# Kernel optimization log

Measured on AMD Instinct MI355X. Metric: run time of the kernel, lower is better.

The kernel has to match this reference:

```python
import jax, jax.numpy as jnp
import numpy as np

B, N, T, C, H, E = 4, 256, 36, 64, 4, 4096
D = C // H          # per-head dim
CH = 2 * C          # GAT hidden channels (embed_size * 2)


def _ln(x, g, b):
    mu = x.mean(-1, keepdims=True)
    v = ((x - mu) ** 2).mean(-1, keepdims=True)
    return (x - mu) / jnp.sqrt(v + 1e-5) * g + b


def _gat_conv(x, src, dst, W, a_s, a_d, b):
    # GATConv, heads=1, add_self_loops=False, negative_slope=0.2
    h = x @ W                                        # [N, F]
    e = jax.nn.leaky_relu((h * a_s).sum(-1)[src] + (h * a_d).sum(-1)[dst], 0.2)  # [E]
    m = jax.ops.segment_max(e, dst, num_segments=N)  # per-dst softmax (stable)
    w = jnp.exp(e - m[dst])
    s = jax.ops.segment_sum(w, dst, num_segments=N)
    alpha = w / (s[dst] + 1e-16)
    return jax.ops.segment_sum(h[src] * alpha[:, None], dst, num_segments=N) + b


def _forward(query, key, value, edge_attr, D_S, W_emb, b_emb, Wq, Wk, Wv, W_fc, b_fc,
             ln1_g, ln1_b, ln2_g, ln2_b, W_ff1, b_ff1, W_ff2, b_ff2,
             gat1_W, gat1_as, gat1_ad, gat1_b, gat2_W, gat2_as, gat2_ad, gat2_b,
             jk_W, jk_b, W_fs, b_fs, W_fg, b_fg, edge_index):
    src, dst = edge_index[0], edge_index[1]

    def gat(x):  # [N, C] -> [N, C]; 2-layer GAT with jk='max'
        h1 = jax.nn.relu(_gat_conv(x, src, dst, gat1_W, gat1_as, gat1_ad, gat1_b))
        h2 = jax.nn.relu(_gat_conv(h1, src, dst, gat2_W, gat2_as, gat2_ad, gat2_b))
        return jnp.maximum(h1, h2) @ jk_W + jk_b

    # GAT is applied to the ORIGINAL query (before D_S is added), once per timestep.
    xg = jax.vmap(jax.vmap(gat))(query.transpose(0, 2, 1, 3))  # [B, T, N, C]
    # source loop PREPENDS each timestep's output -> time axis is reversed
    X_G = xg[:, ::-1].transpose(0, 2, 1, 3)                    # [B, N, T, C]

    ds = (D_S @ W_emb + b_emb)[None, :, None, :]               # [1, N, 1, C]
    q = query + ds
    k = key + ds
    v = value + ds

    qh = q.reshape(B, N, T, H, D) @ Wq                         # per-head shared linear
    kh = k.reshape(B, N, T, H, D) @ Wk
    vh = v.reshape(B, N, T, H, D) @ Wv
    attn = jnp.einsum('bqthd,bkthd->bqkth', qh, kh)            # [B, N, N, T, H]
    # NOTE: source softmaxes over dim=1 (the QUERY axis), scaled by sqrt(embed_size)
    a = jax.nn.softmax(attn / jnp.sqrt(jnp.float32(C)), axis=1)
    o = jnp.einsum('bqkth,bkthd->bqthd', a, vh).reshape(B, N, T, C)
    o = o @ W_fc + b_fc

    M_s = _ln(o + q, ln1_g, ln1_b)                             # dropout p=0 (identity)
    ff = jax.nn.relu(M_s @ W_ff1 + b_ff1) @ W_ff2 + b_ff2
    U_s = _ln(ff + M_s, ln2_g, ln2_b)

    g = jax.nn.sigmoid(U_s @ W_fs + b_fs + X_G @ W_fg + b_fg)
    return g * U_s + (1.0 - g) * X_G


def setup_inputs():
    key = jax.random.key(0)
    ki = iter(jax.random.split(key, 64))

    def p(shape):
        fan = shape[0]
        return jax.random.normal(next(ki), shape, dtype=jnp.float32) / jnp.float32(float(np.sqrt(fan)))

    inp = {}
    inp['query'] = jax.random.normal(next(ki), (B, N, T, C), dtype=jnp.float32)
    inp['key'] = jax.random.normal(next(ki), (B, N, T, C), dtype=jnp.float32)
    inp['value'] = jax.random.normal(next(ki), (B, N, T, C), dtype=jnp.float32)
    inp['edge_attr'] = jax.random.normal(next(ki), (E,), dtype=jnp.float32)
    inp['D_S'] = jax.random.normal(next(ki), (N, N), dtype=jnp.float32)  # adj, learned param
    inp['W_emb'] = p((N, C)); inp['b_emb'] = jnp.zeros((C,), jnp.float32)
    inp['Wq'] = p((D, D)); inp['Wk'] = p((D, D)); inp['Wv'] = p((D, D))
    inp['W_fc'] = p((C, C)); inp['b_fc'] = jnp.zeros((C,), jnp.float32)
    inp['ln1_g'] = jnp.ones((C,), jnp.float32); inp['ln1_b'] = jnp.zeros((C,), jnp.float32)
    inp['ln2_g'] = jnp.ones((C,), jnp.float32); inp['ln2_b'] = jnp.zeros((C,), jnp.float32)
    inp['W_ff1'] = p((C, 4 * C)); inp['b_ff1'] = jnp.zeros((4 * C,), jnp.float32)
    inp['W_ff2'] = p((4 * C, C)); inp['b_ff2'] = jnp.zeros((C,), jnp.float32)
    inp['gat1_W'] = p((C, CH)); inp['gat1_as'] = p((CH,)); inp['gat1_ad'] = p((CH,)); inp['gat1_b'] = jnp.zeros((CH,), jnp.float32)
    inp['gat2_W'] = p((CH, CH)); inp['gat2_as'] = p((CH,)); inp['gat2_ad'] = p((CH,)); inp['gat2_b'] = jnp.zeros((CH,), jnp.float32)
    inp['jk_W'] = p((CH, C)); inp['jk_b'] = jnp.zeros((C,), jnp.float32)
    inp['W_fs'] = p((C, C)); inp['b_fs'] = jnp.zeros((C,), jnp.float32)
    inp['W_fg'] = p((C, C)); inp['b_fg'] = jnp.zeros((C,), jnp.float32)
    inp['edge_index'] = jax.random.randint(next(ki), (2, E), 0, N, dtype=jnp.int32)
    return inp


def reference(query, key, value, edge_attr, D_S, W_emb, b_emb, Wq, Wk, Wv, W_fc, b_fc,
              ln1_g, ln1_b, ln2_g, ln2_b, W_ff1, b_ff1, W_ff2, b_ff2,
              gat1_W, gat1_as, gat1_ad, gat1_b, gat2_W, gat2_as, gat2_ad, gat2_b,
              jk_W, jk_b, W_fs, b_fs, W_fg, b_fg, edge_index):
    return _forward(query, key, value, edge_attr, D_S, W_emb, b_emb, Wq, Wk, Wv, W_fc, b_fc,
                    ln1_g, ln1_b, ln2_g, ln2_b, W_ff1, b_ff1, W_ff2, b_ff2,
                    gat1_W, gat1_as, gat1_ad, gat1_b, gat2_W, gat2_as, gat2_ad, gat2_b,
                    jk_W, jk_b, W_fs, b_fs, W_fg, b_fg, edge_index)
```

## Files before the change

### kernel.cpp

```cpp
#include <hip/hip_runtime.h>

typedef unsigned short u16;
typedef unsigned int u32;

#define B_ 4
#define N_ 256
#define T_ 36
#define C_ 64
#define H_ 4
#define D_ 16
#define CH_ 128
#define E_ 4096
#define EQ_ 1408
#define G_ (B_*T_)
#define TOK_ (B_*N_*T_)

#define DS_OFF  0
#define XG_OFF  (DS_OFF + N_*C_)
#define HA_OFF  (XG_OFF + TOK_*C_)
#define HB_OFF  (HA_OFF + G_*N_*CH_/2)
#define HS_OFF  (HB_OFF + G_*N_*CH_/2)
#define HD_OFF  (HS_OFF + G_*N_)
#define INT_OFF (HD_OFF + G_*N_)
#define MS_OFF  (INT_OFF + 4608)
#define O_SEP_OFF (MS_OFF + 576*512)

__device__ __forceinline__ float bf2f(u16 u){
  u32 x = ((u32)u) << 16;
  return __builtin_bit_cast(float, x);
}
__device__ __forceinline__ u16 f2bf(float f){
  u32 x = __builtin_bit_cast(u32, f);
  x += 0x7fffu + ((x >> 16) & 1u);
  return (u16)(x >> 16);
}
__device__ __forceinline__ void unpack8(uint4 u, float* f){
  f[0]=bf2f((u16)(u.x & 0xffffu)); f[1]=bf2f((u16)(u.x >> 16));
  f[2]=bf2f((u16)(u.y & 0xffffu)); f[3]=bf2f((u16)(u.y >> 16));
  f[4]=bf2f((u16)(u.z & 0xffffu)); f[5]=bf2f((u16)(u.z >> 16));
  f[6]=bf2f((u16)(u.w & 0xffffu)); f[7]=bf2f((u16)(u.w >> 16));
}
__device__ __forceinline__ uint4 pack8f(const float* f){
  uint4 u;
  u.x = (u32)f2bf(f[0]) | ((u32)f2bf(f[1]) << 16);
  u.y = (u32)f2bf(f[2]) | ((u32)f2bf(f[3]) << 16);
  u.z = (u32)f2bf(f[4]) | ((u32)f2bf(f[5]) << 16);
  u.w = (u32)f2bf(f[6]) | ((u32)f2bf(f[7]) << 16);
  return u;
}
__device__ __forceinline__ int rfl(int v){ return __builtin_amdgcn_readfirstlane(v); }

__device__ __forceinline__ void gq_from_bid(int bid, int& g, int& q){
  int xc = bid & 7, slot = bid >> 3;
  q = slot & 3;
  g = xc + ((slot >> 2) << 3);
}

#define SP_ 20

__device__ __forceinline__ void edge_softmax_par(int tid, int n0,
    const int* __restrict__ indptr, int p00,
    const int* srcs_l, const float* hs_l, const float* __restrict__ hd_ws,
    int g, float* alpha_l)
{
  const int ld = tid >> 2;
  const int sl = tid & 3;
  const int dst = n0 + ld;
  const int p0 = indptr[dst] - p00, p1 = indptr[dst+1] - p00;
  const float hdn = hd_ws[g*N_ + dst];
  float m = -1e30f;
  for (int j = p0 + sl; j < p1; j += 4){
    float e = hs_l[srcs_l[j]] + hdn;
    e = e > 0.f ? e : 0.2f * e;
    alpha_l[j] = e;
    m = fmaxf(m, e);
  }
  m = fmaxf(m, __shfl_xor(m, 1, 64));
  m = fmaxf(m, __shfl_xor(m, 2, 64));
  float s = 0.f;
  for (int j = p0 + sl; j < p1; j += 4){
    float w = __expf(alpha_l[j] - m);
    alpha_l[j] = w; s += w;
  }
  s += __shfl_xor(s, 1, 64);
  s += __shfl_xor(s, 2, 64);
  float inv = 1.f / (s + 1e-16f);
  for (int j = p0 + sl; j < p1; j += 4) alpha_l[j] *= inv;
}

__global__ __launch_bounds__(256)
void k_pre(const float* __restrict__ query, const float* __restrict__ W1,
           const float* __restrict__ as1, const float* __restrict__ ad1,
           u16* __restrict__ h, float* __restrict__ hs_ws, float* __restrict__ hd_ws,
           const float* __restrict__ DSm, const float* __restrict__ Wemb,
           const float* __restrict__ bemb, float* __restrict__ dsb,
           const int* __restrict__ ei, int* __restrict__ indptr, int* __restrict__ srcs)
{
  __shared__ union UP {
    struct { float xs[64][65]; float red[2][4][64]; } lin;
    struct { int srcL[E_]; int dstL[E_]; int tmp[E_]; int cnt[N_]; int base[N_+1]; } c;
  } S;
  const int bid = blockIdx.x;
  const int tid = threadIdx.x;

  if (bid < 576){
    int g, q; gq_from_bid(bid, g, q);
    const int n0 = q * 64;
    const int b = g / T_, t = g % T_;
    {
      const size_t gb = (((size_t)b*N_ + n0)*T_ + t)*C_;
      #pragma unroll
      for (int it = 0; it < 4; it++){
        int idx = tid + 256*it;
        int row = idx >> 4, c4 = (idx & 15) * 4;
        float4 v = *(const float4*)(query + gb + (size_t)row*(T_*C_) + c4);
        S.lin.xs[row][c4+0] = v.x; S.lin.xs[row][c4+1] = v.y;
        S.lin.xs[row][c4+2] = v.z; S.lin.xs[row][c4+3] = v.w;
      }
    }
    __syncthreads();

    const int r = tid & 63;
    const int cb = rfl(tid >> 6);
    const int ch0 = cb * 32;

    float acc[32];
    #pragma unroll
    for (int j = 0; j < 32; j++) acc[j] = 0.f;
    for (int k = 0; k < 64; k++){
      float xv = S.lin.xs[r][k];
      const float* wrow = W1 + k*CH_ + ch0;
      #pragma unroll
      for (int j = 0; j < 32; j++) acc[j] += xv * wrow[j];
    }
    float hs = 0.f, hd = 0.f;
    #pragma unroll
    for (int j = 0; j < 32; j++){ hs += acc[j]*as1[ch0+j]; hd += acc[j]*ad1[ch0+j]; }
    S.lin.red[0][cb][r] = hs; S.lin.red[1][cb][r] = hd;

    u16* hp = h + ((size_t)(g*N_ + n0 + r))*CH_ + ch0;
    #pragma unroll
    for (int j8 = 0; j8 < 32; j8 += 8)
      *(uint4*)(hp + j8) = pack8f(&acc[j8]);

    __syncthreads();
    if (tid < 64){
      float a = S.lin.red[0][0][tid]+S.lin.red[0][1][tid]+S.lin.red[0][2][tid]+S.lin.red[0][3][tid];
      float d = S.lin.red[1][0][tid]+S.lin.red[1][1][tid]+S.lin.red[1][2][tid]+S.lin.red[1][3][tid];
      hs_ws[g*N_ + n0 + tid] = a;
      hd_ws[g*N_ + n0 + tid] = d;
    }
  } else if (bid < 640){
    const int n = (bid - 576) * 4 + (tid >> 6);
    const int c = tid & 63;
    float acc = bemb[c];
    for (int m = 0; m < N_; m++) acc += DSm[n*N_ + m] * Wemb[m*C_ + c];
    dsb[n*C_ + c] = acc;
  } else {
    for (int e = tid; e < E_; e += 256){ S.c.srcL[e] = ei[e]; S.c.dstL[e] = ei[E_ + e]; }
    S.c.cnt[tid] = 0;
    __syncthreads();
    for (int e = tid; e < E_; e += 256) atomicAdd(&S.c.cnt[S.c.dstL[e]], 1);
    __syncthreads();
    if (tid == 0){
      int run = 0;
      for (int i = 0; i < N_; i++){ S.c.base[i] = run; run += S.c.cnt[i]; }
      S.c.base[N_] = run;
    }
    __syncthreads();
    S.c.cnt[tid] = 0;
    __syncthreads();
    for (int e = tid; e < E_; e += 256){
      int d = S.c.dstL[e];
      int p = atomicAdd(&S.c.cnt[d], 1);
      S.c.tmp[S.c.base[d] + p] = e;
    }
    __syncthreads();
    {
      const int p0 = S.c.base[tid], p1 = S.c.base[tid] + S.c.cnt[tid];
      for (int i = p0 + 1; i < p1; i++){
        int v = S.c.tmp[i]; int j = i - 1;
        while (j >= p0 && S.c.tmp[j] > v){ S.c.tmp[j+1] = S.c.tmp[j]; j--; }
        S.c.tmp[j+1] = v;
      }
      for (int j = p0; j < p1; j++) srcs[j] = S.c.srcL[S.c.tmp[j]];
    }
    indptr[tid] = S.c.base[tid];
    if (tid == 0) indptr[N_] = S.c.base[N_];
  }
}

__global__ __launch_bounds__(256)
void k_agg1stat(const u16* __restrict__ hin, const float* __restrict__ hs_ws, const float* __restrict__ hd_ws,
                const int* __restrict__ indptr, const int* __restrict__ srcs,
                const float* __restrict__ bias, u16* __restrict__ hout,
                const float* __restrict__ query, const float* __restrict__ key,
                const float* __restrict__ Wq, const float* __restrict__ Wk,
                const float* __restrict__ dsb, float* __restrict__ mS)
{
  __shared__ union UA {
    struct { int srcs_l[EQ_]; float alpha_l[EQ_]; float hs_l[N_]; } a;
    struct { float qs[N_][SP_]; float wq[16][16]; float wk[16][16]; } s;
  } U;
  const int bid = blockIdx.x;
  const int tid = threadIdx.x;

  if (bid < 576){
    int g, q; gq_from_bid(bid, g, q);
    const int n0 = q * 64;

    const int p00 = indptr[n0];
    const int pend = indptr[n0 + 64];
    const int cntE = pend - p00;
    for (int i = tid; i < cntE; i += 256) U.a.srcs_l[i] = srcs[p00 + i];
    U.a.hs_l[tid] = hs_ws[g*N_ + tid];
    __syncthreads();

    edge_softmax_par(tid, n0, indptr, p00, U.a.srcs_l, U.a.hs_l, hd_ws, g, U.a.alpha_l);
    __syncthreads();

    const int r = tid & 63;
    const int cb = rfl(tid >> 6);
    const int ch0 = cb * 32;
    const int dst = n0 + r;
    const int p0 = indptr[dst] - p00, p1 = indptr[dst+1] - p00;

    float acc[32];
    #pragma unroll
    for (int j = 0; j < 32; j++) acc[j] = 0.f;
    for (int j = p0; j < p1; j++){
      float a = U.a.alpha_l[j];
      int s = U.a.srcs_l[j];
      const uint4* hp = (const uint4*)(hin + ((size_t)(g*N_ + s))*CH_ + ch0);
      #pragma unroll
      for (int qq = 0; qq < 4; qq++){
        float hv[8]; unpack8(hp[qq], hv);
        #pragma unroll
        for (int i = 0; i < 8; i++) acc[qq*8+i] += a * hv[i];
      }
    }
    float o[32];
    #pragma unroll
    for (int j = 0; j < 32; j++){
      float v = acc[j] + bias[ch0+j];
      o[j] = v > 0.f ? v : 0.f;
    }
    u16* op = hout + ((size_t)(g*N_ + dst))*CH_ + ch0;
    #pragma unroll
    for (int j8 = 0; j8 < 32; j8 += 8)
      *(uint4*)(op + j8) = pack8f(&o[j8]);
  } else {
    const int sb = bid - 576;
    const int b = sb / (T_*H_);
    const int rem = sb % (T_*H_);
    const int t = rem / H_;
    const int h = rem % H_;
    const int n = tid;

    U.s.wq[n>>4][n&15] = Wq[n];
    U.s.wk[n>>4][n&15] = Wk[n];

    const size_t base = ((((size_t)b*N_ + n)*T_) + t)*C_ + h*D_;
    const float* dsp = dsb + n*C_ + h*D_;

    float x[16];
    #pragma unroll
    for (int j4 = 0; j4 < 16; j4 += 4){
      float4 a = *(const float4*)(query + base + j4);
      float4 d = *(const float4*)(dsp + j4);
      x[j4]=a.x+d.x; x[j4+1]=a.y+d.y; x[j4+2]=a.z+d.z; x[j4+3]=a.w+d.w;
    }
    __syncthreads();
    #pragma unroll
    for (int j = 0; j < 16; j++){
      float a = 0.f;
      #pragma unroll
      for (int i = 0; i < 16; i++) a += x[i]*U.s.wq[i][j];
      U.s.qs[n][j] = a;
    }
    float khr[16];
    #pragma unroll
    for (int j4 = 0; j4 < 16; j4 += 4){
      float4 a = *(const float4*)(key + base + j4);
      float4 d = *(const float4*)(dsp + j4);
      x[j4]=a.x+d.x; x[j4+1]=a.y+d.y; x[j4+2]=a.z+d.z; x[j4+3]=a.w+d.w;
    }
    #pragma unroll
    for (int j = 0; j < 16; j++){
      float a = 0.f;
      #pragma unroll
      for (int i = 0; i < 16; i++) a += x[i]*U.s.wk[i][j];
      khr[j] = a;
    }
    __syncthreads();

    float m[4], s[4];
    #pragma unroll
    for (int c = 0; c < 4; c++){ m[c] = -1e30f; s[c] = 0.f; }
    for (int qq = 0; qq < 64; qq++){
      #pragma unroll
      for (int c = 0; c < 4; c++){
        const float* qrow = &U.s.qs[qq + 64*c][0];
        float4 a0 = *(const float4*)(qrow);
        float4 a1 = *(const float4*)(qrow+4);
        float4 a2 = *(const float4*)(qrow+8);
        float4 a3 = *(const float4*)(qrow+12);
        float d = a0.x*khr[0]+a0.y*khr[1]+a0.z*khr[2]+a0.w*khr[3]
                + a1.x*khr[4]+a1.y*khr[5]+a1.z*khr[6]+a1.w*khr[7]
                + a2.x*khr[8]+a2.y*khr[9]+a2.z*khr[10]+a2.w*khr[11]
                + a3.x*khr[12]+a3.y*khr[13]+a3.z*khr[14]+a3.w*khr[15];
        d *= 0.125f;
        float mn = fmaxf(m[c], d);
        s[c] = s[c]*__expf(m[c]-mn) + __expf(d-mn);
        m[c] = mn;
      }
    }
    float M = fmaxf(fmaxf(m[0],m[1]), fmaxf(m[2],m[3]));
    float S = s[0]*__expf(m[0]-M) + s[1]*__expf(m[1]-M)
            + s[2]*__expf(m[2]-M) + s[3]*__expf(m[3]-M);
    mS[(size_t)sb*512 + n*2]     = M;
    mS[(size_t)sb*512 + n*2 + 1] = 1.f / S;
  }
}

__global__ __launch_bounds__(256)
void k_lin2(const u16* __restrict__ h1, const float* __restrict__ W2,
            const float* __restrict__ as2, const float* __restrict__ ad2,
            u16* __restrict__ h2, float* __restrict__ hs_ws, float* __restrict__ hd_ws)
{
  __shared__ float xs[64][129];
  __shared__ float red[2][4][64];
  const int bid = blockIdx.x;
  int g, q; gq_from_bid(bid, g, q);
  const int n0 = q * 64;
  const int tid = threadIdx.x;

  {
    #pragma unroll
    for (int it = 0; it < 4; it++){
      int idx = tid + 256*it;
      int row = idx >> 4, c8 = (idx & 15) * 8;
      uint4 u = *(const uint4*)(h1 + ((size_t)(g*N_ + n0 + row))*CH_ + c8);
      float v[8]; unpack8(u, v);
      #pragma unroll
      for (int i = 0; i < 8; i++) xs[row][c8+i] = v[i];
    }
  }
  __syncthreads();

  const int r = tid & 63;
  const int cb = rfl(tid >> 6);
  const int ch0 = cb * 32;

  float acc[32];
  #pragma unroll
  for (int j = 0; j < 32; j++) acc[j] = 0.f;
  for (int k = 0; k < 128; k++){
    float xv = xs[r][k];
    const float* wrow = W2 + k*CH_ + ch0;
    #pragma unroll
    for (int j = 0; j < 32; j++) acc[j] += xv * wrow[j];
  }
  float hs = 0.f, hd = 0.f;
  #pragma unroll
  for (int j = 0; j < 32; j++){ hs += acc[j]*as2[ch0+j]; hd += acc[j]*ad2[ch0+j]; }
  red[0][cb][r] = hs; red[1][cb][r] = hd;

  u16* hp = h2 + ((size_t)(g*N_ + n0 + r))*CH_ + ch0;
  #pragma unroll
  for (int j8 = 0; j8 < 32; j8 += 8)
    *(uint4*)(hp + j8) = pack8f(&acc[j8]);

  __syncthreads();
  if (tid < 64){
    float a = red[0][0][tid]+red[0][1][tid]+red[0][2][tid]+red[0][3][tid];
    float d = red[1][0][tid]+red[1][1][tid]+red[1][2][tid]+red[1][3][tid];
    hs_ws[g*N_ + n0 + tid] = a;
    hd_ws[g*N_ + n0 + tid] = d;
  }
}

__global__ __launch_bounds__(256)
void k_agg2av(const u16* __restrict__ h2, const float* __restrict__ hs_ws, const float* __restrict__ hd_ws,
              const int* __restrict__ indptr, const int* __restrict__ srcs,
              const float* __restrict__ b2, const u16* __restrict__ h1,
              const float* __restrict__ jkW, const float* __restrict__ jkb, float* __restrict__ xg,
              const float* __restrict__ query, const float* __restrict__ key, const float* __restrict__ value,
              const float* __restrict__ Wq, const float* __restrict__ Wk, const float* __restrict__ Wv,
              const float* __restrict__ dsb, const float* __restrict__ mS, float* __restrict__ o_ws,
              int bid_base)
{
  __shared__ union UJ {
    struct { int srcs_l[EQ_]; float alpha_l[EQ_]; float hs_l[N_]; } a;
    struct { u16 xs[64][136]; } l;
    struct { float ks[N_][SP_]; float vs[N_][SP_]; float2 msl[N_];
             float wq[16][16]; float wk[16][16]; float wv[16][16]; } v;
  } U;
  const int bid = blockIdx.x + bid_base;
  const int tid = threadIdx.x;

  if (bid < 576){
    int g, q; gq_from_bid(bid, g, q);
    const int n0 = q * 64;
    const int b = g / T_, t = g % T_;

    const int p00 = indptr[n0];
    const int pend = indptr[n0 + 64];
    const int cntE = pend - p00;
    for (int i = tid; i < cntE; i += 256) U.a.srcs_l[i] = srcs[p00 + i];
    U.a.hs_l[tid] = hs_ws[g*N_ + tid];
    __syncthreads();

    edge_softmax_par(tid, n0, indptr, p00, U.a.srcs_l, U.a.hs_l, hd_ws, g, U.a.alpha_l);
    __syncthreads();

    const int r = tid & 63;
    const int cb = rfl(tid >> 6);
    const int ch0 = cb * 32;
    const int dst = n0 + r;
    const int p0 = indptr[dst] - p00, p1 = indptr[dst+1] - p00;

    float acc[32];
    #pragma unroll
    for (int j = 0; j < 32; j++) acc[j] = 0.f;
    for (int j = p0; j < p1; j++){
      float a = U.a.alpha_l[j];
      int s = U.a.srcs_l[j];
      const uint4* hp = (const uint4*)(h2 + ((size_t)(g*N_ + s))*CH_ + ch0);
      #pragma unroll
      for (int qq = 0; qq < 4; qq++){
        float hv[8]; unpack8(hp[qq], hv);
        #pragma unroll
        for (int i = 0; i < 8; i++) acc[qq*8+i] += a * hv[i];
      }
    }
    float o[32];
    {
      const uint4* h1p = (const uint4*)(h1 + ((size_t)(g*N_ + dst))*CH_ + ch0);
      #pragma unroll
      for (int j8 = 0; j8 < 32; j8 += 8){
        float h1v[8]; unpack8(h1p[j8>>3], h1v);
        #pragma unroll
        for (int i = 0; i < 8; i++){
          float v = acc[j8+i] + b2[ch0+j8+i];
          v = v > 0.f ? v : 0.f;
          o[j8+i] = fmaxf(h1v[i], v);
        }
      }
    }
    __syncthreads();

    #pragma unroll
    for (int j8 = 0; j8 < 32; j8 += 8)
      *(uint4*)&U.l.xs[r][ch0 + j8] = pack8f(&o[j8]);
    __syncthreads();

    const int o0 = cb * 16;
    float acc2[16];
    #pragma unroll
    for (int j = 0; j < 16; j++) acc2[j] = 0.f;
    for (int k8 = 0; k8 < 16; k8++){
      uint4 u = *(const uint4*)&U.l.xs[r][k8*8];
      float hv[8]; unpack8(u, hv);
      #pragma unroll
      for (int kk = 0; kk < 8; kk++){
        const float* wrow = jkW + (k8*8+kk)*C_ + o0;
        #pragma unroll
        for (int j = 0; j < 16; j++) acc2[j] += hv[kk] * wrow[j];
      }
    }
    float* op = xg + ((((size_t)b*N_ + n0 + r)*T_) + (T_-1-t))*C_ + o0;
    #pragma unroll
    for (int j4 = 0; j4 < 16; j4 += 4){
      float4 v = make_float4(acc2[j4]+jkb[o0+j4], acc2[j4+1]+jkb[o0+j4+1],
                             acc2[j4+2]+jkb[o0+j4+2], acc2[j4+3]+jkb[o0+j4+3]);
      *(float4*)(op + j4) = v;
    }
  } else {
    const int sb = bid - 576;
    const int b = sb / (T_*H_);
    const int rem = sb % (T_*H_);
    const int t = rem / H_;
    const int h = rem % H_;
    const int n = tid;

    U.v.wq[n>>4][n&15] = Wq[n];
    U.v.wk[n>>4][n&15] = Wk[n];
    U.v.wv[n>>4][n&15] = Wv[n];
    U.v.msl[n] = *(const float2*)(mS + (size_t)sb*512 + n*2);

    const size_t base = ((((size_t)b*N_ + n)*T_) + t)*C_ + h*D_;
    const float* dsp = dsb + n*C_ + h*D_;

    float ds16[16];
    #pragma unroll
    for (int j4 = 0; j4 < 16; j4 += 4){
      float4 d = *(const float4*)(dsp + j4);
      ds16[j4]=d.x; ds16[j4+1]=d.y; ds16[j4+2]=d.z; ds16[j4+3]=d.w;
    }
    __syncthreads();

    float x[16];
    #pragma unroll
    for (int j4 = 0; j4 < 16; j4 += 4){
      float4 a = *(const float4*)(key + base + j4);
      x[j4]=a.x+ds16[j4]; x[j4+1]=a.y+ds16[j4+1]; x[j4+2]=a.z+ds16[j4+2]; x[j4+3]=a.w+ds16[j4+3];
    }
    #pragma unroll
    for (int j = 0; j < 16; j++){
      float a = 0.f;
      #pragma unroll
      for (int i = 0; i < 16; i++) a += x[i]*U.v.wk[i][j];
      U.v.ks[n][j] = a;
    }
    #pragma unroll
    for (int j4 = 0; j4 < 16; j4 += 4){
      float4 a = *(const float4*)(value + base + j4);
      x[j4]=a.x+ds16[j4]; x[j4+1]=a.y+ds16[j4+1]; x[j4+2]=a.z+ds16[j4+2]; x[j4+3]=a.w+ds16[j4+3];
    }
    #pragma unroll
    for (int j = 0; j < 16; j++){
      float a = 0.f;
      #pragma unroll
      for (int i = 0; i < 16; i++) a += x[i]*U.v.wv[i][j];
      U.v.vs[n][j] = a;
    }
    float qhr[16];
    #pragma unroll
    for (int j4 = 0; j4 < 16; j4 += 4){
      float4 a = *(const float4*)(query + base + j4);
      x[j4]=a.x+ds16[j4]; x[j4+1]=a.y+ds16[j4+1]; x[j4+2]=a.z+ds16[j4+2]; x[j4+3]=a.w+ds16[j4+3];
    }
    #pragma unroll
    for (int j = 0; j < 16; j++){
      float a = 0.f;
      #pragma unroll
      for (int i = 0; i < 16; i++) a += x[i]*U.v.wq[i][j];
      qhr[j] = a;
    }
    __syncthreads();

    float o0[16], o1[16];
    #pragma unroll
    for (int j = 0; j < 16; j++){ o0[j] = 0.f; o1[j] = 0.f; }
    for (int k = 0; k < N_; k += 2){
      {
        const float* krow = &U.v.ks[k][0];
        float4 a0 = *(const float4*)(krow);
        float4 a1 = *(const float4*)(krow+4);
        float4 a2 = *(const float4*)(krow+8);
        float4 a3 = *(const float4*)(krow+12);
        float d = a0.x*qhr[0]+a0.y*qhr[1]+a0.z*qhr[2]+a0.w*qhr[3]
                + a1.x*qhr[4]+a1.y*qhr[5]+a1.z*qhr[6]+a1.w*qhr[7]
                + a2.x*qhr[8]+a2.y*qhr[9]+a2.z*qhr[10]+a2.w*qhr[11]
                + a3.x*qhr[12]+a3.y*qhr[13]+a3.z*qhr[14]+a3.w*qhr[15];
        float2 ms0 = U.v.msl[k];
        float p = __expf(d*0.125f - ms0.x) * ms0.y;
        const float* vrow = &U.v.vs[k][0];
        float4 v0 = *(const float4*)(vrow);
        float4 v1 = *(const float4*)(vrow+4);
        float4 v2 = *(const float4*)(vrow+8);
        float4 v3 = *(const float4*)(vrow+12);
        o0[0]+=p*v0.x; o0[1]+=p*v0.y; o0[2]+=p*v0.z; o0[3]+=p*v0.w;
        o0[4]+=p*v1.x; o0[5]+=p*v1.y; o0[6]+=p*v1.z; o0[7]+=p*v1.w;
        o0[8]+=p*v2.x; o0[9]+=p*v2.y; o0[10]+=p*v2.z; o0[11]+=p*v2.w;
        o0[12]+=p*v3.x; o0[13]+=p*v3.y; o0[14]+=p*v3.z; o0[15]+=p*v3.w;
      }
      {
        const float* krow = &U.v.ks[k+1][0];
        float4 a0 = *(const float4*)(krow);
        float4 a1 = *(const float4*)(krow+4);
        float4 a2 = *(const float4*)(krow+8);
        float4 a3 = *(const float4*)(krow+12);
        float d = a0.x*qhr[0]+a0.y*qhr[1]+a0.z*qhr[2]+a0.w*qhr[3]
                + a1.x*qhr[4]+a1.y*qhr[5]+a1.z*qhr[6]+a1.w*qhr[7]
                + a2.x*qhr[8]+a2.y*qhr[9]+a2.z*qhr[10]+a2.w*qhr[11]
                + a3.x*qhr[12]+a3.y*qhr[13]+a3.z*qhr[14]+a3.w*qhr[15];
        float2 ms1 = U.v.msl[k+1];
        float p = __expf(d*0.125f - ms1.x) * ms1.y;
        const float* vrow = &U.v.vs[k+1][0];
        float4 v0 = *(const float4*)(vrow);
        float4 v1 = *(const float4*)(vrow+4);
        float4 v2 = *(const float4*)(vrow+8);
        float4 v3 = *(const float4*)(vrow+12);
        o1[0]+=p*v0.x; o1[1]+=p*v0.y; o1[2]+=p*v0.z; o1[3]+=p*v0.w;
        o1[4]+=p*v1.x; o1[5]+=p*v1.y; o1[6]+=p*v1.z; o1[7]+=p*v1.w;
        o1[8]+=p*v2.x; o1[9]+=p*v2.y; o1[10]+=p*v2.z; o1[11]+=p*v2.w;
        o1[12]+=p*v3.x; o1[13]+=p*v3.y; o1[14]+=p*v3.z; o1[15]+=p*v3.w;
      }
    }
    float* op = o_ws + base;
    #pragma unroll
    for (int j4 = 0; j4 < 16; j4 += 4)
      *(float4*)(op + j4) = make_float4(o0[j4]+o1[j4], o0[j4+1]+o1[j4+1],
                                        o0[j4+2]+o1[j4+2], o0[j4+3]+o1[j4+3]);
  }
}

__global__ __launch_bounds__(256)
void k_final(const float* __restrict__ query, const float* __restrict__ dsb,
             const float* __restrict__ o_ws, const float* __restrict__ xg_ws,
             const float* __restrict__ Wfc, const float* __restrict__ bfc,
             const float* __restrict__ ln1g, const float* __restrict__ ln1b,
             const float* __restrict__ ln2g, const float* __restrict__ ln2b,
             const float* __restrict__ Wff1, const float* __restrict__ bff1,
             const float* __restrict__ Wff2, const float* __restrict__ bff2,
             const float* __restrict__ Wfs, const float* __restrict__ bfs,
             const float* __restrict__ Wfg, const float* __restrict__ bfg,
             float* __restrict__ out)
{
  __shared__ u16 smA[64*66];
  __shared__ u16 smB[64*66];
  __shared__ union UH { u16 h[128*66]; float o[64*66]; } HH;
  __shared__ float lnxA[4][64];
  __shared__ float lnxB[4][64];

  const int tid = threadIdx.x;
  const int token0 = blockIdx.x * 64;
  const int w = rfl(tid >> 6);
  const int tok = tid & 63;
  const int c0 = w * 16;

  #pragma unroll
  for (int it = 0; it < 4; it++){
    int idx = tid + 256*it;
    int tk = idx >> 4, c4 = (idx & 15) * 4;
    int gtok = token0 + tk;
    int n = (gtok / T_) & (N_-1);
    float4 ov = *(const float4*)(o_ws + (size_t)gtok*C_ + c4);
    float4 qv = *(const float4*)(query + (size_t)gtok*C_ + c4);
    float4 dv = *(const float4*)(dsb + n*C_ + c4);
    smA[(c4+0)*66+tk] = f2bf(ov.x); smA[(c4+1)*66+tk] = f2bf(ov.y);
    smA[(c4+2)*66+tk] = f2bf(ov.z); smA[(c4+3)*66+tk] = f2bf(ov.w);
    smB[(c4+0)*66+tk] = f2bf(qv.x+dv.x); smB[(c4+1)*66+tk] = f2bf(qv.y+dv.y);
    smB[(c4+2)*66+tk] = f2bf(qv.z+dv.z); smB[(c4+3)*66+tk] = f2bf(qv.w+dv.w);
  }
  __syncthreads();

  float x1[16];
  #pragma unroll
  for (int j = 0; j < 16; j++) x1[j] = 0.f;
  for (int i = 0; i < C_; i++){
    float ov = bf2f(smA[i*66 + tok]);
    const float* wrow = Wfc + i*C_ + c0;
    #pragma unroll
    for (int j = 0; j < 16; j++) x1[j] += ov * wrow[j];
  }
  #pragma unroll
  for (int j = 0; j < 16; j++) x1[j] += bfc[c0+j] + bf2f(smB[(c0+j)*66 + tok]);

  float s1 = 0.f;
  #pragma unroll
  for (int j = 0; j < 16; j++) s1 += x1[j];
  lnxA[w][tok] = s1;
  __syncthreads();
  float mu = (lnxA[0][tok]+lnxA[1][tok]+lnxA[2][tok]+lnxA[3][tok]) * (1.f/64.f);
  float v1 = 0.f;
  #pragma unroll
  for (int j = 0; j < 16; j++){ float d = x1[j]-mu; v1 += d*d; }
  lnxB[w][tok] = v1;
  __syncthreads();
  float var = (lnxB[0][tok]+lnxB[1][tok]+lnxB[2][tok]+lnxB[3][tok]) * (1.f/64.f);
  float rstd = rsqrtf(var + 1e-5f);
  float ms[16];
  #pragma unroll
  for (int j = 0; j < 16; j++) ms[j] = (x1[j]-mu)*rstd*ln1g[c0+j] + ln1b[c0+j];
  __syncthreads();
  #pragma unroll
  for (int j = 0; j < 16; j++) smB[(c0+j)*66 + tok] = f2bf(ms[j]);
  __syncthreads();

  float part[16];
  #pragma unroll
  for (int j = 0; j < 16; j++) part[j] = 0.f;
  #pragma unroll
  for (int ch = 0; ch < 2; ch++){
    float fch[32];
    #pragma unroll
    for (int kk = 0; kk < 32; kk++) fch[kk] = 0.f;
    const int kbase = w*64 + ch*32;
    for (int i = 0; i < C_; i++){
      float msv = bf2f(smB[i*66 + tok]);
      const float* wrow = Wff1 + i*(4*C_) + kbase;
      #pragma unroll
      for (int kk = 0; kk < 32; kk++) fch[kk] += msv * wrow[kk];
    }
    #pragma unroll
    for (int kk = 0; kk < 32; kk++){
      float v = fch[kk] + bff1[kbase+kk];
      fch[kk] = v > 0.f ? v : 0.f;
    }
    if (ch) __syncthreads();
    #pragma unroll
    for (int kk = 0; kk < 32; kk++) HH.h[(w*32+kk)*66 + tok] = f2bf(fch[kk]);
    __syncthreads();
    #pragma unroll
    for (int wq = 0; wq < 4; wq++){
      #pragma unroll 8
      for (int kk = 0; kk < 32; kk++){
        int k = wq*64 + ch*32 + kk;
        float hv = bf2f(HH.h[(wq*32+kk)*66 + tok]);
        const float* wrow = Wff2 + k*C_ + c0;
        #pragma unroll
        for (int j = 0; j < 16; j++) part[j] += hv * wrow[j];
      }
    }
  }
  float x2[16];
  #pragma unroll
  for (int j = 0; j < 16; j++) x2[j] = part[j] + bff2[c0+j] + ms[j];

  float s2 = 0.f;
  #pragma unroll
  for (int j = 0; j < 16; j++) s2 += x2[j];
  __syncthreads();
  lnxA[w][tok] = s2;
  __syncthreads();
  float mu2 = (lnxA[0][tok]+lnxA[1][tok]+lnxA[2][tok]+lnxA[3][tok]) * (1.f/64.f);
  float v2 = 0.f;
  #pragma unroll
  for (int j = 0; j < 16; j++){ float d = x2[j]-mu2; v2 += d*d; }
  lnxB[w][tok] = v2;
  __syncthreads();
  float var2 = (lnxB[0][tok]+lnxB[1][tok]+lnxB[2][tok]+lnxB[3][tok]) * (1.f/64.f);
  float rstd2 = rsqrtf(var2 + 1e-5f);
  float us[16];
  #pragma unroll
  for (int j = 0; j < 16; j++) us[j] = (x2[j]-mu2)*rstd2*ln2g[c0+j] + ln2b[c0+j];

  #pragma unroll
  for (int j = 0; j < 16; j++) smA[(c0+j)*66 + tok] = f2bf(us[j]);
  #pragma unroll
  for (int it = 0; it < 4; it++){
    int idx = tid + 256*it;
    int tk = idx >> 4, c4 = (idx & 15) * 4;
    int gtok = token0 + tk;
    float4 xv = *(const float4*)(xg_ws + (size_t)gtok*C_ + c4);
    HH.h[(c4+0)*66+tk] = f2bf(xv.x); HH.h[(c4+1)*66+tk] = f2bf(xv.y);
    HH.h[(c4+2)*66+tk] = f2bf(xv.z); HH.h[(c4+3)*66+tk] = f2bf(xv.w);
  }
  __syncthreads();

  float ga[16];
  #pragma unroll
  for (int j = 0; j < 16; j++) ga[j] = 0.f;
  for (int i = 0; i < C_; i++){
    float uv = bf2f(smA[i*66 + tok]);
    float xv = bf2f(HH.h[i*66 + tok]);
    const float* wsr = Wfs + i*C_ + c0;
    const float* wgr = Wfg + i*C_ + c0;
    #pragma unroll
    for (int j = 0; j < 16; j++) ga[j] += uv*wsr[j] + xv*wgr[j];
  }
  float res[16];
  #pragma unroll
  for (int j = 0; j < 16; j++){
    float a = ga[j] + bfs[c0+j] + bfg[c0+j];
    float gg = 1.f / (1.f + __expf(-a));
    float xgv = bf2f(HH.h[(c0+j)*66 + tok]);
    res[j] = gg*us[j] + (1.f-gg)*xgv;
  }
  __syncthreads();
  #pragma unroll
  for (int j = 0; j < 16; j++) HH.o[(c0+j)*66 + tok] = res[j];
  __syncthreads();
  #pragma unroll
  for (int it = 0; it < 4; it++){
    int idx = tid + 256*it;
    int tk = idx >> 4, c4 = (idx & 15) * 4;
    int gtok = token0 + tk;
    float4 v = make_float4(HH.o[(c4+0)*66+tk], HH.o[(c4+1)*66+tk],
                           HH.o[(c4+2)*66+tk], HH.o[(c4+3)*66+tk]);
    *(float4*)(out + (size_t)gtok*C_ + c4) = v;
  }
}

extern "C" void kernel_launch(void* const* d_in, const int* in_sizes, int n_in,
                              void* d_out, int out_size, void* d_ws, size_t ws_size,
                              hipStream_t stream)
{
  (void)in_sizes; (void)n_in; (void)out_size;
  const float* query = (const float*)d_in[0];
  const float* key   = (const float*)d_in[1];
  const float* value = (const float*)d_in[2];
  const float* DSm   = (const float*)d_in[4];
  const float* Wemb  = (const float*)d_in[5];
  const float* bemb  = (const float*)d_in[6];
  const float* Wq    = (const float*)d_in[7];
  const float* Wk    = (const float*)d_in[8];
  const float* Wv    = (const float*)d_in[9];
  const float* Wfc   = (const float*)d_in[10];
  const float* bfc   = (const float*)d_in[11];
  const float* ln1g  = (const float*)d_in[12];
  const float* ln1b  = (const float*)d_in[13];
  const float* ln2g  = (const float*)d_in[14];
  const float* ln2b  = (const float*)d_in[15];
  const float* Wff1  = (const float*)d_in[16];
  const float* bff1  = (const float*)d_in[17];
  const float* Wff2  = (const float*)d_in[18];
  const float* bff2  = (const float*)d_in[19];
  const float* g1W   = (const float*)d_in[20];
  const float* g1as  = (const float*)d_in[21];
  const float* g1ad  = (const float*)d_in[22];
  const float* g1b   = (const float*)d_in[23];
  const float* g2W   = (const float*)d_in[24];
  const float* g2as  = (const float*)d_in[25];
  const float* g2ad  = (const float*)d_in[26];
  const float* g2b   = (const float*)d_in[27];
  const float* jkW   = (const float*)d_in[28];
  const float* jkb   = (const float*)d_in[29];
  const float* Wfs   = (const float*)d_in[30];
  const float* bfs   = (const float*)d_in[31];
  const float* Wfg   = (const float*)d_in[32];
  const float* bfg   = (const float*)d_in[33];
  const int* ei      = (const int*)d_in[34];
  float* out = (float*)d_out;

  float* wf     = (float*)d_ws;
  float* dsb    = wf + DS_OFF;
  float* xg_ws  = wf + XG_OFF;
  u16*   hA     = (u16*)(wf + HA_OFF);
  u16*   hB     = (u16*)(wf + HB_OFF);
  float* hs_ws  = wf + HS_OFF;
  float* hd_ws  = wf + HD_OFF;
  int*   indptr = (int*)(wf + INT_OFF);
  int*   srcs   = indptr + 260;
  float* mS     = wf + MS_OFF;

  const size_t need = (size_t)(O_SEP_OFF + TOK_*C_) * 4;
  const bool sep = ws_size >= need;
  float* o_ws = sep ? (wf + O_SEP_OFF) : (wf + HA_OFF);

  k_pre     <<<dim3(641),  dim3(256), 0, stream>>>(query, g1W, g1as, g1ad, hA, hs_ws, hd_ws,
                                                   DSm, Wemb, bemb, dsb, ei, indptr, srcs);
  k_agg1stat<<<dim3(1152), dim3(256), 0, stream>>>(hA, hs_ws, hd_ws, indptr, srcs, g1b, hB,
                                                   query, key, Wq, Wk, dsb, mS);
  k_lin2    <<<dim3(576),  dim3(256), 0, stream>>>(hB, g2W, g2as, g2ad, hA, hs_ws, hd_ws);
  if (sep){
    k_agg2av<<<dim3(1152), dim3(256), 0, stream>>>(hA, hs_ws, hd_ws, indptr, srcs, g2b, hB,
                                                   jkW, jkb, xg_ws,
                                                   query, key, value, Wq, Wk, Wv, dsb, mS, o_ws, 0);
  } else {
    k_agg2av<<<dim3(576),  dim3(256), 0, stream>>>(hA, hs_ws, hd_ws, indptr, srcs, g2b, hB,
                                                   jkW, jkb, xg_ws,
                                                   query, key, value, Wq, Wk, Wv, dsb, mS, o_ws, 0);
    k_agg2av<<<dim3(576),  dim3(256), 0, stream>>>(hA, hs_ws, hd_ws, indptr, srcs, g2b, hB,
                                                   jkW, jkb, xg_ws,
                                                   query, key, value, Wq, Wk, Wv, dsb, mS, o_ws, 576);
  }
  k_final   <<<dim3(576),  dim3(256), 0, stream>>>(query, dsb, o_ws, xg_ws,
      Wfc, bfc, ln1g, ln1b, ln2g, ln2b,
      Wff1, bff1, Wff2, bff2,
      Wfs, bfs, Wfg, bfg, out);
}
```

Before: 280.0 us.

## Prefetch next edge row in GAT gather and store attention K/V as bf16

The GAT aggregation loops now go through a helper that loads the next source row's features and alpha while the current row is accumulated, hiding gather latency. The attention path's K and V tiles in shared memory move from fp32 padded rows to packed 16-bit rows (bf16 via pack8f) and are unpacked on read. This halves the shared-memory footprint and LDS traffic, which can raise occupancy. The cost is lower precision in K/V and extra unpack ALU work, plus more registers held by the prefetch buffers.

```diff
diff --git a/kernel.cpp b/kernel.cpp
--- a/kernel.cpp
+++ b/kernel.cpp
@@ -88,6 +88,44 @@
   for (int j = p0 + sl; j < p1; j += 4) alpha_l[j] *= inv;
 }
 
+__device__ __forceinline__ void gather_pipelined(
+    const u16* __restrict__ hin, int gN, int ch0,
+    const int* srcs_l, const float* alpha_l, int p0, int p1, float* acc)
+{
+  uint4 c0v, c1v, c2v, c3v;
+  float aC = 0.f;
+  if (p0 < p1){
+    int s = srcs_l[p0];
+    const uint4* hp = (const uint4*)(hin + ((size_t)(gN + s))*CH_ + ch0);
+    c0v = hp[0]; c1v = hp[1]; c2v = hp[2]; c3v = hp[3];
+    aC = alpha_l[p0];
+  }
+  for (int j = p0; j < p1; j++){
+    uint4 n0v = c0v, n1v = c1v, n2v = c2v, n3v = c3v;
+    float aN = aC;
+    if (j + 1 < p1){
+      int s = srcs_l[j+1];
+      const uint4* hp = (const uint4*)(hin + ((size_t)(gN + s))*CH_ + ch0);
+      n0v = hp[0]; n1v = hp[1]; n2v = hp[2]; n3v = hp[3];
+      aN = alpha_l[j+1];
+    }
+    float hv[8];
+    unpack8(c0v, hv);
+    #pragma unroll
+    for (int i = 0; i < 8; i++) acc[i] += aC * hv[i];
+    unpack8(c1v, hv);
+    #pragma unroll
+    for (int i = 0; i < 8; i++) acc[8+i] += aC * hv[i];
+    unpack8(c2v, hv);
+    #pragma unroll
+    for (int i = 0; i < 8; i++) acc[16+i] += aC * hv[i];
+    unpack8(c3v, hv);
+    #pragma unroll
+    for (int i = 0; i < 8; i++) acc[24+i] += aC * hv[i];
+    c0v = n0v; c1v = n1v; c2v = n2v; c3v = n3v; aC = aN;
+  }
+}
+
 __global__ __launch_bounds__(256)
 void k_pre(const float* __restrict__ query, const float* __restrict__ W1,
            const float* __restrict__ as1, const float* __restrict__ ad1,
@@ -228,17 +266,8 @@
     float acc[32];
     #pragma unroll
     for (int j = 0; j < 32; j++) acc[j] = 0.f;
-    for (int j = p0; j < p1; j++){
-      float a = U.a.alpha_l[j];
-      int s = U.a.srcs_l[j];
-      const uint4* hp = (const uint4*)(hin + ((size_t)(g*N_ + s))*CH_ + ch0);
-      #pragma unroll
-      for (int qq = 0; qq < 4; qq++){
-        float hv[8]; unpack8(hp[qq], hv);
-        #pragma unroll
-        for (int i = 0; i < 8; i++) acc[qq*8+i] += a * hv[i];
-      }
-    }
+    gather_pipelined(hin, g*N_, ch0, U.a.srcs_l, U.a.alpha_l, p0, p1, acc);
+
     float o[32];
     #pragma unroll
     for (int j = 0; j < 32; j++){
@@ -393,7 +422,7 @@
   __shared__ union UJ {
     struct { int srcs_l[EQ_]; float alpha_l[EQ_]; float hs_l[N_]; } a;
     struct { u16 xs[64][136]; } l;
-    struct { float ks[N_][SP_]; float vs[N_][SP_]; float2 msl[N_];
+    struct { u16 ks[N_][16]; u16 vs[N_][16]; float2 msl[N_];
              float wq[16][16]; float wk[16][16]; float wv[16][16]; } v;
   } U;
   const int bid = blockIdx.x + bid_base;
@@ -423,17 +452,8 @@
     float acc[32];
     #pragma unroll
     for (int j = 0; j < 32; j++) acc[j] = 0.f;
-    for (int j = p0; j < p1; j++){
-      float a = U.a.alpha_l[j];
-      int s = U.a.srcs_l[j];
-      const uint4* hp = (const uint4*)(h2 + ((size_t)(g*N_ + s))*CH_ + ch0);
-      #pragma unroll
-      for (int qq = 0; qq < 4; qq++){
-        float hv[8]; unpack8(hp[qq], hv);
-        #pragma unroll
-        for (int i = 0; i < 8; i++) acc[qq*8+i] += a * hv[i];
-      }
-    }
+    gather_pipelined(h2, g*N_, ch0, U.a.srcs_l, U.a.alpha_l, p0, p1, acc);
+
     float o[32];
     {
       const uint4* h1p = (const uint4*)(h1 + ((size_t)(g*N_ + dst))*CH_ + ch0);
@@ -500,7 +520,7 @@
     }
     __syncthreads();
 
-    float x[16];
+    float x[16], r0[16];
     #pragma unroll
     for (int j4 = 0; j4 < 16; j4 += 4){
       float4 a = *(const float4*)(key + base + j4);
@@ -511,8 +531,11 @@
       float a = 0.f;
       #pragma unroll
       for (int i = 0; i < 16; i++) a += x[i]*U.v.wk[i][j];
-      U.v.ks[n][j] = a;
-    }
+      r0[j] = a;
+    }
+    *(uint4*)&U.v.ks[n][0] = pack8f(&r0[0]);
+    *(uint4*)&U.v.ks[n][8] = pack8f(&r0[8]);
+
     #pragma unroll
     for (int j4 = 0; j4 < 16; j4 += 4){
       float4 a = *(const float4*)(value + base + j4);
@@ -523,8 +546,11 @@
       float a = 0.f;
       #pragma unroll
       for (int i = 0; i < 16; i++) a += x[i]*U.v.wv[i][j];
-      U.v.vs[n][j] = a;
-    }
+      r0[j] = a;
+    }
+    *(uint4*)&U.v.vs[n][0] = pack8f(&r0[0]);
+    *(uint4*)&U.v.vs[n][8] = pack8f(&r0[8]);
+
     float qhr[16];
     #pragma unroll
     for (int j4 = 0; j4 < 16; j4 += 4){
@@ -545,48 +571,36 @@
     for (int j = 0; j < 16; j++){ o0[j] = 0.f; o1[j] = 0.f; }
     for (int k = 0; k < N_; k += 2){
       {
-        const float* krow = &U.v.ks[k][0];
-        float4 a0 = *(const float4*)(krow);
-        float4 a1 = *(const float4*)(krow+4);
-        float4 a2 = *(const float4*)(krow+8);
-        float4 a3 = *(const float4*)(krow+12);
-        float d = a0.x*qhr[0]+a0.y*qhr[1]+a0.z*qhr[2]+a0.w*qhr[3]
-                + a1.x*qhr[4]+a1.y*qhr[5]+a1.z*qhr[6]+a1.w*qhr[7]
-                + a2.x*qhr[8]+a2.y*qhr[9]+a2.z*qhr[10]+a2.w*qhr[11]
-                + a3.x*qhr[12]+a3.y*qhr[13]+a3.z*qhr[14]+a3.w*qhr[15];
+        uint4 u0 = *(const uint4*)&U.v.ks[k][0];
+        uint4 u1 = *(const uint4*)&U.v.ks[k][8];
+        float kv[16]; unpack8(u0, kv); unpack8(u1, kv+8);
+        float d = kv[0]*qhr[0]+kv[1]*qhr[1]+kv[2]*qhr[2]+kv[3]*qhr[3]
+                + kv[4]*qhr[4]+kv[5]*qhr[5]+kv[6]*qhr[6]+kv[7]*qhr[7]
+                + kv[8]*qhr[8]+kv[9]*qhr[9]+kv[10]*qhr[10]+kv[11]*qhr[11]
+                + kv[12]*qhr[12]+kv[13]*qhr[13]+kv[14]*qhr[14]+kv[15]*qhr[15];
         float2 ms0 = U.v.msl[k];
         float p = __expf(d*0.125f - ms0.x) * ms0.y;
-        const float* vrow = &U.v.vs[k][0];
-        float4 v0 = *(const float4*)(vrow);
-        float4 v1 = *(const float4*)(vrow+4);
-        float4 v2 = *(const float4*)(vrow+8);
-        float4 v3 = *(const float4*)(vrow+12);
-        o0[0]+=p*v0.x; o0[1]+=p*v0.y; o0[2]+=p*v0.z; o0[3]+=p*v0.w;
-        o0[4]+=p*v1.x; o0[5]+=p*v1.y; o0[6]+=p*v1.z; o0[7]+=p*v1.w;
-        o0[8]+=p*v2.x; o0[9]+=p*v2.y; o0[10]+=p*v2.z; o0[11]+=p*v2.w;
-        o0[12]+=p*v3.x; o0[13]+=p*v3.y; o0[14]+=p*v3.z; o0[15]+=p*v3.w;
+        uint4 v0 = *(const uint4*)&U.v.vs[k][0];
+        uint4 v1 = *(const uint4*)&U.v.vs[k][8];
+        float vv[16]; unpack8(v0, vv); unpack8(v1, vv+8);
+        #pragma unroll
+        for (int j = 0; j < 16; j++) o0[j] += p * vv[j];
       }
       {
-        const float* krow = &U.v.ks[k+1][0];
-        float4 a0 = *(const float4*)(krow);
-        float4 a1 = *(const float4*)(krow+4);
-        float4 a2 = *(const float4*)(krow+8);
-        float4 a3 = *(const float4*)(krow+12);
-        float d = a0.x*qhr[0]+a0.y*qhr[1]+a0.z*qhr[2]+a0.w*qhr[3]
-                + a1.x*qhr[4]+a1.y*qhr[5]+a1.z*qhr[6]+a1.w*qhr[7]
-                + a2.x*qhr[8]+a2.y*qhr[9]+a2.z*qhr[10]+a2.w*qhr[11]
-                + a3.x*qhr[12]+a3.y*qhr[13]+a3.z*qhr[14]+a3.w*qhr[15];
+        uint4 u0 = *(const uint4*)&U.v.ks[k+1][0];
+        uint4 u1 = *(const uint4*)&U.v.ks[k+1][8];
+        float kv[16]; unpack8(u0, kv); unpack8(u1, kv+8);
+        float d = kv[0]*qhr[0]+kv[1]*qhr[1]+kv[2]*qhr[2]+kv[3]*qhr[3]
+                + kv[4]*qhr[4]+kv[5]*qhr[5]+kv[6]*qhr[6]+kv[7]*qhr[7]
+                + kv[8]*qhr[8]+kv[9]*qhr[9]+kv[10]*qhr[10]+kv[11]*qhr[11]
+                + kv[12]*qhr[12]+kv[13]*qhr[13]+kv[14]*qhr[14]+kv[15]*qhr[15];
         float2 ms1 = U.v.msl[k+1];
         float p = __expf(d*0.125f - ms1.x) * ms1.y;
-        const float* vrow = &U.v.vs[k+1][0];
-        float4 v0 = *(const float4*)(vrow);
-        float4 v1 = *(const float4*)(vrow+4);
-        float4 v2 = *(const float4*)(vrow+8);
-        float4 v3 = *(const float4*)(vrow+12);
-        o1[0]+=p*v0.x; o1[1]+=p*v0.y; o1[2]+=p*v0.z; o1[3]+=p*v0.w;
-        o1[4]+=p*v1.x; o1[5]+=p*v1.y; o1[6]+=p*v1.z; o1[7]+=p*v1.w;
-        o1[8]+=p*v2.x; o1[9]+=p*v2.y; o1[10]+=p*v2.z; o1[11]+=p*v2.w;
-        o1[12]+=p*v3.x; o1[13]+=p*v3.y; o1[14]+=p*v3.z; o1[15]+=p*v3.w;
+        uint4 v0 = *(const uint4*)&U.v.vs[k+1][0];
+        uint4 v1 = *(const uint4*)&U.v.vs[k+1][8];
+        float vv[16]; unpack8(v0, vv); unpack8(v1, vv+8);
+        #pragma unroll
+        for (int j = 0; j < 16; j++) o1[j] += p * vv[j];
       }
     }
     float* op = o_ws + base;
```

Result: slower. 316.2 us (+12.9%).
